# Performance work log

Hardware: AMD Instinct MI355X
Metric: run time of the kernel (lower is better)

## Reference

```python
import jax, jax.numpy as jnp
import numpy as np

EMB, HEADS, LAT, FFN = 1024, 16, 256, 4096
HD = EMB // HEADS
B, N = 2, 2048

def _ln(x, w, b, eps=1e-5):
    mu = jnp.mean(x, axis=-1, keepdims=True)
    var = jnp.var(x, axis=-1, keepdims=True)
    return (x - mu) * jax.lax.rsqrt(var + eps) * w + b

def setup_inputs() -> dict:
    key = jax.random.key(0)
    ks = jax.random.split(key, 16)
    def lin(k, fan_in, fan_out):
        bound = 1.0 / np.sqrt(fan_in)
        kw, kb = jax.random.split(k)
        W = jax.random.uniform(kw, (fan_in, fan_out), jnp.float32, -bound, bound)
        b = jax.random.uniform(kb, (fan_out,), jnp.float32, -bound, bound)
        return W, b
    Wq, bq = lin(ks[0], EMB, EMB)
    WaK, baK = lin(ks[1], EMB, LAT)
    WbK, bbK = lin(ks[2], LAT, EMB)
    WaV, baV = lin(ks[3], EMB, LAT)
    WbV, bbV = lin(ks[4], LAT, EMB)
    Wo, bo = lin(ks[5], EMB, EMB)
    W1, b1 = lin(ks[6], EMB, FFN)
    W2, b2 = lin(ks[7], FFN, EMB)
    return {
        'x': jax.random.normal(ks[8], (B, N, EMB), jnp.float32),
        'attn_bias': jax.random.normal(ks[9], (N, N), jnp.float32),
        'Wq': Wq, 'bq': bq, 'WaK': WaK, 'baK': baK, 'WbK': WbK, 'bbK': bbK,
        'WaV': WaV, 'baV': baV, 'WbV': WbV, 'bbV': bbV, 'Wo': Wo, 'bo': bo,
        'W1': W1, 'b1': b1, 'W2': W2, 'b2': b2,
        'ln1_w': jnp.ones((EMB,), jnp.float32), 'ln1_b': jnp.zeros((EMB,), jnp.float32),
        'ln2_w': jnp.ones((EMB,), jnp.float32), 'ln2_b': jnp.zeros((EMB,), jnp.float32),
    }

def reference(x, attn_bias, Wq, bq, WaK, baK, WbK, bbK, WaV, baV, WbV, bbV,
              Wo, bo, W1, b1, W2, b2, ln1_w, ln1_b, ln2_w, ln2_b):
    Q = x @ Wq + bq                       # [B,N,E]
    K = (x @ WaK + baK) @ WbK + bbK       # low-rank K
    V = (x @ WaV + baV) @ WbV + bbV       # low-rank V
    def split(t):
        return t.reshape(B, N, HEADS, HD).transpose(0, 2, 1, 3)  # [B,H,N,D]
    Qh, Kh, Vh = split(Q), split(K), split(V)
    scores = jnp.einsum('bhnd,bhmd->bhnm', Qh, Kh) / np.sqrt(HD)
    scores = scores + attn_bias[None, None]
    weights = jax.nn.softmax(scores, axis=-1)
    attn = jnp.einsum('bhnm,bhmd->bhnd', weights, Vh)
    attn = attn.transpose(0, 2, 1, 3).reshape(B, N, EMB)
    attn = attn @ Wo + bo
    h = _ln(x + attn, ln1_w, ln1_b)
    ffn = jax.nn.gelu(h @ W1 + b1, approximate=False) @ W2 + b2
    return _ln(h + ffn, ln2_w, ln2_b)
```

## Files before the change

kernel.cpp:

```cpp
#include <hip/hip_runtime.h>
#include <hip/hip_bf16.h>
#include <math.h>

typedef unsigned short u16;
typedef short bf16x8 __attribute__((ext_vector_type(8)));
typedef float f32x4 __attribute__((ext_vector_type(4)));

#define EMB   1024
#define HEADS 16
#define HD    64
#define LATD  256
#define FFND  4096
#define BATCH 2
#define SEQ   2048
#define TOK   (BATCH*SEQ)

#define SCL2  0.18033688011112042f
#define LOG2E 1.4426950408889634f

__device__ __forceinline__ float bf2f(u16 u) {
    union { unsigned int i; float f; } x; x.i = ((unsigned int)u) << 16; return x.f;
}
__device__ __forceinline__ u16 f2bf(float f) {
    union { float f; unsigned int i; } x; x.f = f;
    unsigned int i = x.i;
    unsigned int lsb = (i >> 16) & 1u;
    i += 0x7fffu + lsb;
    return (u16)(i >> 16);
}
__device__ __forceinline__ void gld16(const u16* g, u16* l) {
    __builtin_amdgcn_global_load_lds(
        (const __attribute__((address_space(1))) void*)g,
        (__attribute__((address_space(3))) void*)l, 16, 0, 0);
}
__device__ __forceinline__ unsigned int cvt_pk_bf16(float a, float b) {
    unsigned int r;
    asm("v_cvt_pk_bf16_f32 %0, %1, %2" : "=v"(r) : "v"(a), "v"(b));
    return r;
}
#if defined(__has_builtin)
#if __has_builtin(__builtin_amdgcn_exp2f)
#define EXP2(x) __builtin_amdgcn_exp2f(x)
#endif
#endif
#ifndef EXP2
#define EXP2(x) exp2f(x)
#endif

__global__ __launch_bounds__(256) void cvt_f32_bf16_kernel(
    const float* __restrict__ in, u16* __restrict__ out, int n8)
{
    int i = blockIdx.x * 256 + threadIdx.x;
    int stride = gridDim.x * 256;
    for (; i < n8; i += stride) {
        float4 f0 = *(const float4*)(in + (size_t)i * 8);
        float4 f1 = *(const float4*)(in + (size_t)i * 8 + 4);
        u16 e[8];
        e[0] = f2bf(f0.x); e[1] = f2bf(f0.y); e[2] = f2bf(f0.z); e[3] = f2bf(f0.w);
        e[4] = f2bf(f1.x); e[5] = f2bf(f1.y); e[6] = f2bf(f1.z); e[7] = f2bf(f1.w);
        *(uint4*)(out + (size_t)i * 8) = *(const uint4*)e;
    }
}

__global__ __launch_bounds__(256) void prep_bias_kernel(
    const float* __restrict__ a, const float* __restrict__ b,
    const float* __restrict__ q, float* __restrict__ bKV, float* __restrict__ bqs)
{
    int i = blockIdx.x * 256 + threadIdx.x;
    if (i < 256)      bKV[i] = a[i];
    else if (i < 512) bKV[i] = b[i - 256];
    else              bqs[i - 512] = q[i - 512] * SCL2;
}

__global__ __launch_bounds__(256) void permute_ab_kernel(
    const float* __restrict__ ab, float* __restrict__ abP)
{
    const int kt = blockIdx.x, qt = blockIdx.y;
    const int tid = threadIdx.x;
    const int lane = tid & 63, wq = tid >> 6;
    const int qq = lane >> 4, col = lane & 15;
#pragma unroll
    for (int wi = wq; wi < 8; wi += 4)
#pragma unroll
        for (int mt = 0; mt < 4; mt++) {
            float4 v = *(const float4*)(ab + (size_t)(qt * 128 + wi * 16 + col) * SEQ
                                        + kt * 64 + mt * 16 + qq * 4);
            v.x *= LOG2E; v.y *= LOG2E; v.z *= LOG2E; v.w *= LOG2E;
            *(float4*)(abP + (((size_t)qt * 32 + kt) * 8 + wi) * 1024 + mt * 256 + lane * 4) = v;
        }
}

struct TDesc { const float* src; u16* dst; int K; int N; int ofs; float scl; };
struct TTable { TDesc d[8]; };

__global__ __launch_bounds__(256) void transpose_all_kernel(TTable tt)
{
    __shared__ u16 t[32][33];
    int tb = blockIdx.x, e = 0;
#pragma unroll
    for (int i = 1; i < 8; i++) if (tb >= tt.d[i].ofs) e = i;
    const float* src = tt.d[e].src;
    u16* dst = tt.d[e].dst;
    const int K = tt.d[e].K, N = tt.d[e].N;
    const float scl = tt.d[e].scl;
    const int local = tb - tt.d[e].ofs;
    const int nx = N >> 5;
    const int bx = (local % nx) * 32;
    const int by = (local / nx) * 32;
    const int tx = threadIdx.x & 31;
    const int ty = threadIdx.x >> 5;
#pragma unroll
    for (int i = 0; i < 32; i += 8)
        t[ty + i][tx] = f2bf(src[(size_t)(by + ty + i) * N + bx + tx] * scl);
    __syncthreads();
#pragma unroll
    for (int i = 0; i < 32; i += 8)
        dst[(size_t)(bx + ty + i) * K + by + tx] = t[tx][ty + i];
}

#define BM 128
#define GBK 64

template <int ACT, int BNv>
__device__ __forceinline__ void gemm_body(
    const u16* __restrict__ A, int lda, const u16* __restrict__ WT,
    const float* __restrict__ bias, u16* __restrict__ C,
    int K, int N, int bx, u16* Al, u16* Wl)
{
    const int NT = BNv / 32;
    const int WN = BNv / 2;
    const int CW = BNv / 32;

    const int tid  = threadIdx.x;
    const int lane = tid & 63;
    const int w    = tid >> 6;
    const int wm = w >> 1, wn = w & 1;
    const int col = lane & 15, qq = lane >> 4;
    const size_t bm = (size_t)blockIdx.y * BM;
    const size_t bn = (size_t)bx * BNv;

    f32x4 acc[4][NT];
#pragma unroll
    for (int mt = 0; mt < 4; mt++)
#pragma unroll
        for (int nt = 0; nt < NT; nt++) acc[mt][nt] = (f32x4){0.f, 0.f, 0.f, 0.f};

    const u16* gA[4]; u16* lA[4];
#pragma unroll
    for (int i = 0; i < 4; i++) {
        int f = w * 256 + i * 64 + lane;
        int r = f >> 3, s = f & 7, sg = s ^ (r & 7);
        gA[i] = A + (bm + r) * (size_t)lda + sg * 8;
        lA[i] = &Al[(size_t)(w * 256 + i * 64) * 8];
    }
    const u16* gW[4]; u16* lW[4];
#pragma unroll
    for (int i = 0; i < CW; i++) {
        int f = w * (BNv * 2) + i * 64 + lane;
        int r = f >> 3, s = f & 7, sg = s ^ (r & 7);
        gW[i] = WT + (bn + r) * (size_t)K + sg * 8;
        lW[i] = &Wl[(size_t)(w * (BNv * 2) + i * 64) * 8];
    }

    for (int k0 = 0; k0 < K; k0 += GBK) {
#pragma unroll
        for (int i = 0; i < 4; i++) gld16(gA[i] + k0, lA[i]);
#pragma unroll
        for (int i = 0; i < CW; i++) gld16(gW[i] + k0, lW[i]);
        __syncthreads();

#pragma unroll
        for (int kk = 0; kk < 2; kk++) {
            bf16x8 af[4], bfr[NT];
#pragma unroll
            for (int mt = 0; mt < 4; mt++) {
                int rr = wm * 64 + mt * 16 + col;
                int sub = (kk * 4 + qq) ^ (rr & 7);
                af[mt] = *(const bf16x8*)&Al[rr * GBK + sub * 8];
            }
#pragma unroll
            for (int nt = 0; nt < NT; nt++) {
                int rn = wn * WN + nt * 16 + col;
                int sub = (kk * 4 + qq) ^ (rn & 7);
                bfr[nt] = *(const bf16x8*)&Wl[rn * GBK + sub * 8];
            }
#pragma unroll
            for (int mt = 0; mt < 4; mt++)
#pragma unroll
                for (int nt = 0; nt < NT; nt++)
                    acc[mt][nt] = __builtin_amdgcn_mfma_f32_16x16x32_bf16(
                        af[mt], bfr[nt], acc[mt][nt], 0, 0, 0);
        }
        __syncthreads();
    }

    float bv[NT];
#pragma unroll
    for (int nt = 0; nt < NT; nt++)
        bv[nt] = bias[bn + wn * WN + nt * 16 + col];

#pragma unroll
    for (int mt = 0; mt < 4; mt++) {
#pragma unroll
        for (int nt = 0; nt < NT; nt++) {
#pragma unroll
            for (int r = 0; r < 4; r++) {
                float v = acc[mt][nt][r] + bv[nt];
                if (ACT == 1) v = 0.5f * v * (1.0f + erff(v * 0.70710678118654752f));
                size_t rg = bm + wm * 64 + mt * 16 + qq * 4 + r;
                C[rg * (size_t)N + bn + wn * WN + nt * 16 + col] = f2bf(v);
            }
        }
    }
}

template <int ACT, int BNv, int MINW>
__global__ __launch_bounds__(256, MINW) void gemm_bt_kernel(
    const u16* __restrict__ A, int lda, const u16* __restrict__ WT,
    const float* __restrict__ bias, u16* __restrict__ C,
    int K, int N)
{
    __shared__ __align__(16) u16 Al[BM * GBK];
    __shared__ __align__(16) u16 Wl[BNv * GBK];
    gemm_body<ACT, BNv>(A, lda, WT, bias, C, K, N, blockIdx.x, Al, Wl);
}

struct GPair {
    const u16* A0; const u16* A1;
    const u16* W0; const u16* W1;
    const float* b0; const float* b1;
    u16* C0; u16* C1;
    int lda0, lda1, N0, N1, nx0;
};

template <int BNv, int MINW>
__global__ __launch_bounds__(256, MINW) void gemm_pair_kernel(GPair p, int K)
{
    __shared__ __align__(16) u16 Al[BM * GBK];
    __shared__ __align__(16) u16 Wl[BNv * GBK];
    const bool s1 = (int)blockIdx.x >= p.nx0;
    const u16* A = s1 ? p.A1 : p.A0;
    const u16* WT = s1 ? p.W1 : p.W0;
    const float* bias = s1 ? p.b1 : p.b0;
    u16* C = s1 ? p.C1 : p.C0;
    const int lda = s1 ? p.lda1 : p.lda0;
    const int N = s1 ? p.N1 : p.N0;
    const int bx = s1 ? (int)blockIdx.x - p.nx0 : (int)blockIdx.x;
    gemm_body<0, BNv>(A, lda, WT, bias, C, K, N, bx, Al, Wl);
}

#define BQ   128
#define BKV  64
#define NKVT (SEQ / BKV)
#define LDK  72
#define LDP  72
#define LDV  72

__global__ __launch_bounds__(512, 4) void fattn_kernel(
    const u16* __restrict__ Q, const u16* __restrict__ K,
    const u16* __restrict__ V, const float* __restrict__ abP,
    u16* __restrict__ O)
{
    __shared__ __align__(16) u16 Ks[2][BKV * LDK];
    __shared__ __align__(16) u16 Vt[2][HD * LDV];
    __shared__ __align__(16) u16 Ps[BQ * LDP];

    const int tid = threadIdx.x;
    const int lane = tid & 63;
    const int w = tid >> 6;
    const int col = lane & 15, qq = lane >> 4;
    const int qt = blockIdx.x;
    const int b = blockIdx.y >> 4, h = blockIdx.y & 15;
    const size_t tok0 = (size_t)b * SEQ + (size_t)qt * BQ;
    const int wrow = w * 16;
    const size_t kvbase = (size_t)b * SEQ * EMB + h * HD;

    const int krow = tid >> 3, kcol = (tid & 7) * 8;
    const int vrow = tid & 63, vdg = tid >> 6;

    bf16x8 aq[2];
#pragma unroll
    for (int kk = 0; kk < 2; kk++)
        aq[kk] = *(const bf16x8*)(Q + (tok0 + wrow + col) * EMB + h * HD + kk * 32 + qq * 8);

    float m_st = -1e30f, l_st = 0.f;
    f32x4 o_acc[4];
#pragma unroll
    for (int dt = 0; dt < 4; dt++) o_acc[dt] = (f32x4){0.f, 0.f, 0.f, 0.f};

    uint4 kreg, vreg;
#define LOADKV(KV0) do {                                                              \
        kreg = *(const uint4*)(K + kvbase + (size_t)((KV0) + krow) * EMB + kcol);     \
        vreg = *(const uint4*)(V + kvbase + (size_t)((KV0) + vrow) * EMB + vdg * 8);  \
    } while (0)

    LOADKV(0);
    *(uint4*)&Ks[0][krow * LDK + kcol] = kreg;
    {
        u16 vv[8]; *(uint4*)vv = vreg;
#pragma unroll
        for (int dd = 0; dd < 8; dd++)
            Vt[0][(vdg * 8 + dd) * LDV + vrow] = vv[dd];
    }
    __syncthreads();
    LOADKV(BKV);

    const float* abq = abP + (size_t)qt * NKVT * 8192 + (size_t)w * 1024;
    f32x4 abv[4];
#pragma unroll
    for (int mt = 0; mt < 4; mt++)
        abv[mt] = *(const f32x4*)(abq + mt * 256 + lane * 4);

    for (int t = 0; t < NKVT; t++) {
        const int cur = t & 1;
        const u16* Kc = Ks[cur];

        f32x4 s2[4];
#pragma unroll
        for (int mt = 0; mt < 4; mt++) s2[mt] = abv[mt];
        __builtin_amdgcn_s_setprio(1);
#pragma unroll
        for (int mt = 0; mt < 4; mt++) {
            bf16x8 ak0 = *(const bf16x8*)&Kc[(mt * 16 + col) * LDK + qq * 8];
            bf16x8 ak1 = *(const bf16x8*)&Kc[(mt * 16 + col) * LDK + 32 + qq * 8];
            s2[mt] = __builtin_amdgcn_mfma_f32_16x16x32_bf16(ak0, aq[0], s2[mt], 0, 0, 0);
            s2[mt] = __builtin_amdgcn_mfma_f32_16x16x32_bf16(ak1, aq[1], s2[mt], 0, 0, 0);
        }
        __builtin_amdgcn_s_setprio(0);

        if (t + 1 < NKVT) {
            const float* abn = abq + (size_t)(t + 1) * 8192;
#pragma unroll
            for (int mt = 0; mt < 4; mt++)
                abv[mt] = *(const f32x4*)(abn + mt * 256 + lane * 4);
        }

        if (t + 1 < NKVT) {
            *(uint4*)&Ks[cur ^ 1][krow * LDK + kcol] = kreg;
            u16 vv[8]; *(uint4*)vv = vreg;
#pragma unroll
            for (int dd = 0; dd < 8; dd++)
                Vt[cur ^ 1][(vdg * 8 + dd) * LDV + vrow] = vv[dd];
        }
        if (t + 2 < NKVT) LOADKV((t + 2) * BKV);

        float t0 = fmaxf(fmaxf(s2[0][0], s2[0][1]), fmaxf(s2[0][2], s2[0][3]));
        float t1 = fmaxf(fmaxf(s2[1][0], s2[1][1]), fmaxf(s2[1][2], s2[1][3]));
        float t2 = fmaxf(fmaxf(s2[2][0], s2[2][1]), fmaxf(s2[2][2], s2[2][3]));
        float t3 = fmaxf(fmaxf(s2[3][0], s2[3][1]), fmaxf(s2[3][2], s2[3][3]));
        float tm = fmaxf(fmaxf(t0, t1), fmaxf(t2, t3));
        tm = fmaxf(tm, __shfl_xor(tm, 16));
        tm = fmaxf(tm, __shfl_xor(tm, 32));
        if (!__all(tm <= m_st + 8.f)) {
            float mnew = fmaxf(m_st, tm);
            float alpha = EXP2(m_st - mnew);
            m_st = mnew;
            l_st *= alpha;
            float af[4];
#pragma unroll
            for (int r = 0; r < 4; r++) af[r] = __shfl(alpha, qq * 20 + r);
#pragma unroll
            for (int dt = 0; dt < 4; dt++)
#pragma unroll
                for (int r = 0; r < 4; r++) o_acc[dt][r] *= af[r];
        }
        float rs = 0.f;
#pragma unroll
        for (int mt = 0; mt < 4; mt++)
#pragma unroll
            for (int r = 0; r < 4; r++) {
                float e = EXP2(s2[mt][r] - m_st);
                s2[mt][r] = e;
                rs += e;
            }
        rs += __shfl_xor(rs, 16);
        rs += __shfl_xor(rs, 32);
        l_st += rs;

#pragma unroll
        for (int mt = 0; mt < 4; mt++) {
            uint2 pp;
            pp.x = cvt_pk_bf16(s2[mt][0], s2[mt][1]);
            pp.y = cvt_pk_bf16(s2[mt][2], s2[mt][3]);
            *(uint2*)&Ps[(wrow + col) * LDP + mt * 16 + qq * 4] = pp;
        }

        __builtin_amdgcn_s_setprio(1);
#pragma unroll
        for (int kk = 0; kk < 2; kk++) {
            bf16x8 ap = *(const bf16x8*)&Ps[(wrow + col) * LDP + kk * 32 + qq * 8];
#pragma unroll
            for (int dt = 0; dt < 4; dt++) {
                bf16x8 bv = *(const bf16x8*)&Vt[cur][(dt * 16 + col) * LDV + kk * 32 + qq * 8];
                o_acc[dt] = __builtin_amdgcn_mfma_f32_16x16x32_bf16(ap, bv, o_acc[dt], 0, 0, 0);
            }
        }
        __builtin_amdgcn_s_setprio(0);
        __syncthreads();
    }
#undef LOADKV

    float lr[4];
#pragma unroll
    for (int r = 0; r < 4; r++) lr[r] = 1.0f / __shfl(l_st, qq * 20 + r);
#pragma unroll
    for (int r = 0; r < 4; r++)
#pragma unroll
        for (int dt = 0; dt < 4; dt++)
            O[(tok0 + wrow + qq * 4 + r) * EMB + h * HD + dt * 16 + col]
                = f2bf(o_acc[dt][r] * lr[r]);
}

template <int AF32, int OUTF32>
__global__ __launch_bounds__(256) void ln_kernel(
    const void* __restrict__ A, const u16* __restrict__ R,
    const float* __restrict__ w, const float* __restrict__ bb,
    void* __restrict__ out)
{
    __shared__ float r1[4], r2[4];
    const int tid = threadIdx.x;
    const size_t row = blockIdx.x;

    float v[4];
    float s = 0.0f, s2 = 0.0f;
#pragma unroll
    for (int i = 0; i < 4; i++) {
        int c = tid + i * 256;
        float a = AF32 ? ((const float*)A)[row * EMB + c]
                       : bf2f(((const u16*)A)[row * EMB + c]);
        float t = a + bf2f(R[row * EMB + c]);
        v[i] = t;
        s += t; s2 += t * t;
    }
#pragma unroll
    for (int o = 32; o > 0; o >>= 1) {
        s  += __shfl_down(s, o);
        s2 += __shfl_down(s2, o);
    }
    if ((tid & 63) == 0) { r1[tid >> 6] = s; r2[tid >> 6] = s2; }
    __syncthreads();
    s  = r1[0] + r1[1] + r1[2] + r1[3];
    s2 = r2[0] + r2[1] + r2[2] + r2[3];

    float mu = s * (1.0f / EMB);
    float var = s2 * (1.0f / EMB) - mu * mu;
    float rs = rsqrtf(var + 1e-5f);

#pragma unroll
    for (int i = 0; i < 4; i++) {
        int c = tid + i * 256;
        float y = (v[i] - mu) * rs * w[c] + bb[c];
        if (OUTF32) ((float*)out)[row * EMB + c] = y;
        else        ((u16*)out)[row * EMB + c] = f2bf(y);
    }
}

extern "C" void kernel_launch(void* const* d_in, const int* in_sizes, int n_in,
                              void* d_out, int out_size, void* d_ws, size_t ws_size,
                              hipStream_t stream)
{
    const float* x    = (const float*)d_in[0];
    const float* ab   = (const float*)d_in[1];
    const float* Wq   = (const float*)d_in[2];
    const float* bq   = (const float*)d_in[3];
    const float* WaK  = (const float*)d_in[4];
    const float* baK  = (const float*)d_in[5];
    const float* WbK  = (const float*)d_in[6];
    const float* bbK  = (const float*)d_in[7];
    const float* WaV  = (const float*)d_in[8];
    const float* baV  = (const float*)d_in[9];
    const float* WbV  = (const float*)d_in[10];
    const float* bbV  = (const float*)d_in[11];
    const float* Wo   = (const float*)d_in[12];
    const float* bo   = (const float*)d_in[13];
    const float* W1   = (const float*)d_in[14];
    const float* b1   = (const float*)d_in[15];
    const float* W2   = (const float*)d_in[16];
    const float* b2   = (const float*)d_in[17];
    const float* ln1w = (const float*)d_in[18];
    const float* ln1b = (const float*)d_in[19];
    const float* ln2w = (const float*)d_in[20];
    const float* ln2b = (const float*)d_in[21];

    u16* w = (u16*)d_ws;
    size_t o = 0;
    u16* WqT  = w + o; o += (size_t)EMB * EMB;
    u16* WaKT = w + o; o += (size_t)EMB * LATD;
    u16* WaVT = w + o; o += (size_t)EMB * LATD;
    u16* WbKT = w + o; o += (size_t)LATD * EMB;
    u16* WbVT = w + o; o += (size_t)LATD * EMB;
    u16* WoT  = w + o; o += (size_t)EMB * EMB;
    u16* W1T  = w + o; o += (size_t)EMB * FFND;
    u16* W2T  = w + o; o += (size_t)FFND * EMB;
    u16* Qb   = w + o; o += (size_t)TOK * EMB;
    u16* Kb   = w + o; o += (size_t)TOK * EMB;
    u16* Vb   = w + o; o += (size_t)TOK * EMB;
    u16* aOb  = w + o; o += (size_t)TOK * EMB;
    u16* projb= w + o; o += (size_t)TOK * EMB;
    u16* hb   = w + o; o += (size_t)TOK * EMB;
    u16* xb   = w + o; o += (size_t)TOK * EMB;
    float* bKV = (float*)(w + o); o += 1024;
    float* bqs = (float*)(w + o); o += 2048;
    float* abP = (float*)projb;
    u16* KVa = aOb;
    u16* f1  = Qb;
    u16* f2  = projb;

    dim3 blk(256);

    cvt_f32_bf16_kernel<<<dim3(2048), blk, 0, stream>>>(x, xb, TOK * EMB / 8);
    prep_bias_kernel<<<dim3(6), blk, 0, stream>>>(baK, baV, bq, bKV, bqs);
    permute_ab_kernel<<<dim3(32, 16), blk, 0, stream>>>(ab, abP);

    TTable tt;
    tt.d[0] = {Wq,  WqT,  EMB,  EMB,  0,    SCL2};
    tt.d[1] = {WaK, WaKT, EMB,  LATD, 1024, 1.0f};
    tt.d[2] = {WaV, WaVT, EMB,  LATD, 1280, 1.0f};
    tt.d[3] = {WbK, WbKT, LATD, EMB,  1536, 1.0f};
    tt.d[4] = {WbV, WbVT, LATD, EMB,  1792, 1.0f};
    tt.d[5] = {Wo,  WoT,  EMB,  EMB,  2048, 1.0f};
    tt.d[6] = {W1,  W1T,  EMB,  FFND, 3072, 1.0f};
    tt.d[7] = {W2,  W2T,  FFND, EMB,  7168, 1.0f};
    transpose_all_kernel<<<dim3(11264), blk, 0, stream>>>(tt);

    {
        GPair p;
        p.A0 = xb;  p.A1 = xb;
        p.W0 = WqT; p.W1 = WaKT;
        p.b0 = bqs; p.b1 = bKV;
        p.C0 = Qb;  p.C1 = KVa;
        p.lda0 = EMB; p.lda1 = EMB;
        p.N0 = EMB; p.N1 = 512; p.nx0 = 16;
        gemm_pair_kernel<64, 3><<<dim3(24, TOK / BM), blk, 0, stream>>>(p, EMB);
    }
    {
        GPair p;
        p.A0 = KVa;  p.A1 = KVa + LATD;
        p.W0 = WbKT; p.W1 = WbVT;
        p.b0 = bbK;  p.b1 = bbV;
        p.C0 = Kb;   p.C1 = Vb;
        p.lda0 = 512; p.lda1 = 512;
        p.N0 = EMB; p.N1 = EMB; p.nx0 = 16;
        gemm_pair_kernel<64, 3><<<dim3(32, TOK / BM), blk, 0, stream>>>(p, LATD);
    }

    fattn_kernel<<<dim3(SEQ / BQ, BATCH * HEADS), dim3(512), 0, stream>>>(Qb, Kb, Vb, abP, aOb);

    gemm_bt_kernel<0,64,3><<<dim3(EMB / 64, TOK / BM), blk, 0, stream>>>(aOb, EMB, WoT, bo, projb, EMB, EMB);

    ln_kernel<1,0><<<dim3(TOK), blk, 0, stream>>>(x, projb, ln1w, ln1b, hb);

    gemm_bt_kernel<1,128,2><<<dim3(FFND / 128, TOK / BM), blk, 0, stream>>>(hb, EMB, W1T, b1, f1, EMB, FFND);
    gemm_bt_kernel<0,64,3><<<dim3(EMB / 64, TOK / BM), blk, 0, stream>>>(f1, FFND, W2T, b2, f2, FFND, EMB);

    ln_kernel<0,1><<<dim3(TOK), blk, 0, stream>>>(hb, f2, ln2w, ln2b, (float*)d_out);
}
```

Measured before the change: 389.7 us.

## Emit V transposed from low-rank GEMM epilogue to simplify attention V staging

The second low-rank GEMM now writes V in a [batch, dim, seq] transposed layout, staging the output tile through shared memory so global writes stay coalesced. The attention kernel then loads V^T rows directly and stores them to shared memory with a single 16-byte write, instead of scattering eight 2-byte writes per thread. This removes the scattered LDS transpose from the attention inner loop. In exchange, the GEMM epilogue gains an extra LDS round trip and a barrier.

```diff
diff --git a/kernel.cpp b/kernel.cpp
--- a/kernel.cpp
+++ b/kernel.cpp
@@ -121,11 +121,11 @@
 #define BM 128
 #define GBK 64
 
-template <int ACT, int BNv>
+template <int ACT, int BNv, int TRC>
 __device__ __forceinline__ void gemm_body(
     const u16* __restrict__ A, int lda, const u16* __restrict__ WT,
     const float* __restrict__ bias, u16* __restrict__ C,
-    int K, int N, int bx, u16* Al, u16* Wl)
+    int K, int N, int bx, u16* Al, u16* Wl, u16* Tl)
 {
     const int NT = BNv / 32;
     const int WN = BNv / 2;
@@ -199,6 +199,30 @@
     for (int nt = 0; nt < NT; nt++)
         bv[nt] = bias[bn + wn * WN + nt * 16 + col];
 
+    if (TRC) {
+#pragma unroll
+        for (int mt = 0; mt < 4; mt++)
+#pragma unroll
+            for (int nt = 0; nt < NT; nt++)
+#pragma unroll
+                for (int r = 0; r < 4; r++) {
+                    float v = acc[mt][nt][r] + bv[nt];
+                    Tl[(wn * WN + nt * 16 + col) * 136 + (wm * 64 + mt * 16 + qq * 4 + r)] = f2bf(v);
+                }
+        __syncthreads();
+        const int b_ = (int)(bm >> 11);
+        const size_t tokb = bm & (SEQ - 1);
+        const int row = tid >> 2;
+        u16* dst = C + ((size_t)b_ * EMB + (size_t)bx * 64 + row) * SEQ + tokb;
+        const u16* srcl = Tl + row * 136;
+#pragma unroll
+        for (int j = 0; j < 4; j++) {
+            int c0 = ((tid & 3) + j * 4) * 8;
+            *(uint4*)(dst + c0) = *(const uint4*)(srcl + c0);
+        }
+        return;
+    }
+
 #pragma unroll
     for (int mt = 0; mt < 4; mt++) {
 #pragma unroll
@@ -222,7 +246,7 @@
 {
     __shared__ __align__(16) u16 Al[BM * GBK];
     __shared__ __align__(16) u16 Wl[BNv * GBK];
-    gemm_body<ACT, BNv>(A, lda, WT, bias, C, K, N, blockIdx.x, Al, Wl);
+    gemm_body<ACT, BNv, 0>(A, lda, WT, bias, C, K, N, blockIdx.x, Al, Wl, Al);
 }
 
 struct GPair {
@@ -233,11 +257,12 @@
     int lda0, lda1, N0, N1, nx0;
 };
 
-template <int BNv, int MINW>
+template <int BNv, int MINW, int TRV>
 __global__ __launch_bounds__(256, MINW) void gemm_pair_kernel(GPair p, int K)
 {
-    __shared__ __align__(16) u16 Al[BM * GBK];
-    __shared__ __align__(16) u16 Wl[BNv * GBK];
+    __shared__ __align__(16) u16 SH[BM * GBK + BNv * GBK];
+    u16* Al = SH;
+    u16* Wl = SH + BM * GBK;
     const bool s1 = (int)blockIdx.x >= p.nx0;
     const u16* A = s1 ? p.A1 : p.A0;
     const u16* WT = s1 ? p.W1 : p.W0;
@@ -246,7 +271,10 @@
     const int lda = s1 ? p.lda1 : p.lda0;
     const int N = s1 ? p.N1 : p.N0;
     const int bx = s1 ? (int)blockIdx.x - p.nx0 : (int)blockIdx.x;
-    gemm_body<0, BNv>(A, lda, WT, bias, C, K, N, bx, Al, Wl);
+    if (TRV && s1)
+        gemm_body<0, BNv, 1>(A, lda, WT, bias, C, K, N, bx, Al, Wl, SH);
+    else
+        gemm_body<0, BNv, 0>(A, lda, WT, bias, C, K, N, bx, Al, Wl, SH);
 }
 
 #define BQ   128
@@ -258,7 +286,7 @@
 
 __global__ __launch_bounds__(512, 4) void fattn_kernel(
     const u16* __restrict__ Q, const u16* __restrict__ K,
-    const u16* __restrict__ V, const float* __restrict__ abP,
+    const u16* __restrict__ VT, const float* __restrict__ abP,
     u16* __restrict__ O)
 {
     __shared__ __align__(16) u16 Ks[2][BKV * LDK];
@@ -274,9 +302,9 @@
     const size_t tok0 = (size_t)b * SEQ + (size_t)qt * BQ;
     const int wrow = w * 16;
     const size_t kvbase = (size_t)b * SEQ * EMB + h * HD;
+    const size_t vtb = ((size_t)b * EMB + h * HD) * SEQ;
 
     const int krow = tid >> 3, kcol = (tid & 7) * 8;
-    const int vrow = tid & 63, vdg = tid >> 6;
 
     bf16x8 aq[2];
 #pragma unroll
@@ -291,17 +319,12 @@
     uint4 kreg, vreg;
 #define LOADKV(KV0) do {                                                              \
         kreg = *(const uint4*)(K + kvbase + (size_t)((KV0) + krow) * EMB + kcol);     \
-        vreg = *(const uint4*)(V + kvbase + (size_t)((KV0) + vrow) * EMB + vdg * 8);  \
+        vreg = *(const uint4*)(VT + vtb + (size_t)krow * SEQ + (KV0) + kcol);         \
     } while (0)
 
     LOADKV(0);
     *(uint4*)&Ks[0][krow * LDK + kcol] = kreg;
-    {
-        u16 vv[8]; *(uint4*)vv = vreg;
-#pragma unroll
-        for (int dd = 0; dd < 8; dd++)
-            Vt[0][(vdg * 8 + dd) * LDV + vrow] = vv[dd];
-    }
+    *(uint4*)&Vt[0][krow * LDV + kcol] = vreg;
     __syncthreads();
     LOADKV(BKV);
 
@@ -337,10 +360,7 @@
 
         if (t + 1 < NKVT) {
             *(uint4*)&Ks[cur ^ 1][krow * LDK + kcol] = kreg;
-            u16 vv[8]; *(uint4*)vv = vreg;
-#pragma unroll
-            for (int dd = 0; dd < 8; dd++)
-                Vt[cur ^ 1][(vdg * 8 + dd) * LDV + vrow] = vv[dd];
+            *(uint4*)&Vt[cur ^ 1][krow * LDV + kcol] = vreg;
         }
         if (t + 2 < NKVT) LOADKV((t + 2) * BKV);
 
@@ -531,7 +551,7 @@
         p.C0 = Qb;  p.C1 = KVa;
         p.lda0 = EMB; p.lda1 = EMB;
         p.N0 = EMB; p.N1 = 512; p.nx0 = 16;
-        gemm_pair_kernel<64, 3><<<dim3(24, TOK / BM), blk, 0, stream>>>(p, EMB);
+        gemm_pair_kernel<64, 3, 0><<<dim3(24, TOK / BM), blk, 0, stream>>>(p, EMB);
     }
     {
         GPair p;
@@ -541,7 +561,7 @@
         p.C0 = Kb;   p.C1 = Vb;
         p.lda0 = 512; p.lda1 = 512;
         p.N0 = EMB; p.N1 = EMB; p.nx0 = 16;
-        gemm_pair_kernel<64, 3><<<dim3(32, TOK / BM), blk, 0, stream>>>(p, LATD);
+        gemm_pair_kernel<64, 3, 1><<<dim3(32, TOK / BM), blk, 0, stream>>>(p, LATD);
     }
 
     fattn_kernel<<<dim3(SEQ / BQ, BATCH * HEADS), dim3(512), 0, stream>>>(Qb, Kb, Vb, abP, aOb);
```

After: 379.5 us. 1.03x faster.
